# Optimization experiments

Measured on AMD Instinct MI355X. Metric: run time of the kernel, lower is better.

Reference implementation:

```python
import jax, jax.numpy as jnp
import numpy as np

B, N, D = 8, 1024, 256
H, DK, DV = 8, 64, 64
NEG = -1.0e9


def setup_inputs() -> dict:
    key = jax.random.key(0)
    ks = jax.random.split(key, 8)
    node_features = jax.random.normal(ks[0], (B, N, D), dtype=jnp.float32)
    em = (jax.random.uniform(ks[1], (B, 1, N, N)) < 0.03).astype(jnp.float32)
    eye = jnp.eye(N, dtype=jnp.float32)[None, None]
    edge_mask = jnp.maximum(em, eye)
    distance_weights = jax.random.uniform(ks[2], (B, N), dtype=jnp.float32)
    s = 1.0 / np.sqrt(D)
    Wq = jax.random.normal(ks[3], (D, H * DK), dtype=jnp.float32) * s
    Wk = jax.random.normal(ks[4], (D, H * DK), dtype=jnp.float32) * s
    Wv = jax.random.normal(ks[5], (D, H * DV), dtype=jnp.float32) * s
    Wo = jax.random.normal(ks[6], (H * DV, D), dtype=jnp.float32) / np.sqrt(H * DV)
    bo = jnp.zeros((D,), dtype=jnp.float32)
    return {"node_features": node_features, "edge_mask": edge_mask,
            "distance_weights": distance_weights,
            "Wq": Wq, "Wk": Wk, "Wv": Wv, "Wo": Wo, "bo": bo}


def reference(node_features, edge_mask, distance_weights, Wq, Wk, Wv, Wo, bo):
    b, n, d = node_features.shape
    # project and split heads: [B, H, N, dk]
    q = (node_features @ Wq).reshape(b, n, H, DK).transpose(0, 2, 1, 3)
    k = (node_features @ Wk).reshape(b, n, H, DK).transpose(0, 2, 1, 3)
    v = (node_features @ Wv).reshape(b, n, H, DV).transpose(0, 2, 1, 3)
    # scaled dot-product logits [B, H, N, N]
    logits = jnp.einsum('bhsd,bhtd->bhst', q, k) / jnp.sqrt(jnp.float32(DK))
    # additive edge-mask bias (masked pairs pushed to -1e9)
    logits = logits + (1.0 - edge_mask) * NEG
    # multiplicative per-key distance modulation
    logits = logits * distance_weights[:, None, None, :]
    w = jax.nn.softmax(logits, axis=-1)
    out = jnp.einsum('bhst,bhtd->bhsd', w, v)
    out = out.transpose(0, 2, 1, 3).reshape(b, n, H * DV)
    return out @ Wo + bo
```

## Files before the change

### kernel.cpp

```cpp
#include <hip/hip_runtime.h>
#include <hip/hip_bf16.h>
#include <hip/hip_fp16.h>
#include <cstdint>

#define B_ 8
#define N_ 1024
#define D_ 256
#define H_ 8
#define HD_ 512

typedef _Float16 f16;
typedef _Float16 f16x8 __attribute__((ext_vector_type(8)));
typedef _Float16 f16x4 __attribute__((ext_vector_type(4)));
typedef float f32x4 __attribute__((ext_vector_type(4)));
typedef unsigned long long ull;
typedef unsigned long long ull2 __attribute__((ext_vector_type(2)));

__device__ __forceinline__ void gload16(const void* g, void* l) {
    __builtin_amdgcn_global_load_lds(
        (const __attribute__((address_space(1))) unsigned int*)(uintptr_t)g,
        (__attribute__((address_space(3))) unsigned int*)(uintptr_t)l,
        16, 0, 0);
}

__global__ __launch_bounds__(256) void pack_mask_kernel(
    const float* __restrict__ mask, ull* __restrict__ bmT)
{
    const int wv = threadIdx.x >> 6, lane = threadIdx.x & 63;
    const int r = blockIdx.x * 4 + wv;
    const int b = r >> 10, n = r & 1023;
    const float* row = mask + ((size_t)b * N_ + n) * N_;
    for (int tt = 0; tt < 16; ++tt) {
        float v = row[tt * 64 + lane];
        ull m = __ballot(v != 0.0f);
        if (lane == 0) bmT[((size_t)b * 16 + tt) * N_ + n] = m;
    }
}

__global__ __launch_bounds__(256) void wconv_qkv_kernel(
    const float* __restrict__ Wq, const float* __restrict__ Wk,
    const float* __restrict__ Wv, f16* __restrict__ WT)
{
    __shared__ float Ws[64][65];
    const int tid = threadIdx.x;
    const int c0 = blockIdx.x * 64, k0 = blockIdx.y * 64;
    const int m = c0 >> 9, cw0 = c0 & 511;
    const float* Wsel = (m == 0) ? Wq : (m == 1) ? Wk : Wv;
    const int rr = tid >> 6, cc = tid & 63;
    for (int i = 0; i < 16; ++i)
        Ws[i * 4 + rr][cc] = Wsel[(size_t)(k0 + i * 4 + rr) * HD_ + cw0 + cc];
    __syncthreads();
    for (int i = 0; i < 16; ++i)
        WT[(size_t)(c0 + i * 4 + rr) * D_ + k0 + cc] = (f16)Ws[cc][i * 4 + rr];
}

__global__ __launch_bounds__(256) void wconv_o_kernel(
    const float* __restrict__ Wo, f16* __restrict__ WToT)
{
    __shared__ float Ws[64][65];
    const int tid = threadIdx.x;
    const int c0 = blockIdx.x * 64, k0 = blockIdx.y * 64;
    const int rr = tid >> 6, cc = tid & 63;
    for (int i = 0; i < 16; ++i)
        Ws[i * 4 + rr][cc] = Wo[(size_t)(k0 + i * 4 + rr) * D_ + c0 + cc];
    __syncthreads();
    for (int i = 0; i < 16; ++i)
        WToT[(size_t)(c0 + i * 4 + rr) * HD_ + k0 + cc] = (f16)Ws[cc][i * 4 + rr];
}

__global__ __launch_bounds__(256, 4) void qkv_kernel(
    const float* __restrict__ X, const f16* __restrict__ WT,
    f16* __restrict__ Qh, f16* __restrict__ Kh, f16* __restrict__ Vt)
{
    __shared__ f16 Wsh[256 * 64];
    const int tid = threadIdx.x;
    const int wv = tid >> 6, lane = tid & 63;
    const int g = lane >> 4, li = lane & 15;
    const int row0 = blockIdx.x * 64;
    const int c0 = blockIdx.y * 256;
    const int m = c0 >> 9, cw0 = c0 & 511;

    f32x4 acc[16] = {};
    const float* Xrow = X + (size_t)(row0 + wv * 16 + li) * D_;

    for (int ks = 0; ks < 4; ++ks) {
        __syncthreads();
        for (int i = 0; i < 8; ++i) {
            const int idx = i * 256 + wv * 64 + lane;
            const int c = idx >> 3, ch = idx & 7;
            const f16* src = WT + (size_t)(c0 + c) * D_ + ks * 64 + ((ch ^ (c & 7)) * 8);
            gload16(src, &Wsh[(i * 256 + wv * 64) * 8]);
        }
        __syncthreads();
        for (int kk = 0; kk < 2; ++kk) {
            const int k0 = ks * 64 + kk * 32;
            f32x4 a0 = *reinterpret_cast<const f32x4*>(Xrow + k0 + g * 8);
            f32x4 a1 = *reinterpret_cast<const f32x4*>(Xrow + k0 + g * 8 + 4);
            f16x8 af;
            for (int j = 0; j < 4; ++j) { af[j] = (f16)a0[j]; af[4 + j] = (f16)a1[j]; }
            for (int fc = 0; fc < 16; ++fc) {
                const int c = fc * 16 + li;
                const int chn = (kk * 4 + g) ^ (c & 7);
                f16x8 bf = *reinterpret_cast<const f16x8*>(&Wsh[c * 64 + chn * 8]);
                acc[fc] = __builtin_amdgcn_mfma_f32_16x16x32_f16(af, bf, acc[fc], 0, 0, 0);
            }
        }
    }
    const int b = row0 >> 10;
    const int nloc = (row0 & 1023) + wv * 16 + g * 4;
    for (int fc = 0; fc < 16; ++fc) {
        int cw = cw0 + fc * 16 + li;
        int h = cw >> 6, dk = cw & 63;
        if (m < 2) {
            f16* dst = (m == 0 ? Qh : Kh) + ((size_t)(b * H_ + h) * N_ + nloc) * 64 + dk;
            for (int j = 0; j < 4; ++j) dst[(size_t)j * 64] = (f16)acc[fc][j];
        } else {
            f16x4 v4;
            for (int j = 0; j < 4; ++j) v4[j] = (f16)acc[fc][j];
            *reinterpret_cast<f16x4*>(Vt + ((size_t)(b * H_ + h) * 64 + dk) * N_ + nloc) = v4;
        }
    }
}

__global__ __launch_bounds__(256, 4) void attn_kernel(
    const f16* __restrict__ Qh, const f16* __restrict__ Kh,
    const f16* __restrict__ Vt,
    const ull* __restrict__ bm, const float* __restrict__ dw,
    f16* __restrict__ AO)
{
    __shared__ f16 Ksh[2][4096];
    __shared__ f16 Vsh[2][4096];
    __shared__ f16 Ps[4][1024];
    const int tid = threadIdx.x;
    const int wv = tid >> 6, lane = tid & 63;
    const int g = lane >> 4, li = lane & 15;
    const int bid = (blockIdx.x & 7) * 128 + (blockIdx.x >> 3);
    const int st = bid & 15, h = (bid >> 4) & 7, b = bid >> 7;
    const int s0 = st * 64 + wv * 16;

    const f16* Qbase = Qh + (size_t)(b * H_ + h) * N_ * 64;
    const f16* Kbase = Kh + (size_t)(b * H_ + h) * N_ * 64;
    const f16* Vbase = Vt + (size_t)(b * H_ + h) * 64 * N_;
    const ull* bmb = bm + (size_t)b * 16 * N_;
    const float* dwb = dw + b * N_;

    f16x8 qf[2];
    qf[0] = *reinterpret_cast<const f16x8*>(Qbase + (size_t)(s0 + li) * 64 + g * 8);
    qf[1] = *reinterpret_cast<const f16x8*>(Qbase + (size_t)(s0 + li) * 64 + 32 + g * 8);

    f32x4 of[4] = {};
    float m_run[4], l_run[4];
    for (int j = 0; j < 4; ++j) { m_run[j] = -1e30f; l_run[j] = 0.f; }

    auto stage = [&](int tt, int bf) {
        for (int i = 0; i < 2; ++i) {
            const int idx = i * 256 + wv * 64 + lane;
            const int row = idx >> 3, ch = idx & 7;
            const int sch = (ch ^ (row & 7)) * 8;
            const f16* ksrc = Kbase + (size_t)(tt * 64 + row) * 64 + sch;
            gload16(ksrc, &Ksh[bf][(i * 256 + wv * 64) * 8]);
            const f16* vsrc = Vbase + (size_t)row * N_ + tt * 64 + sch;
            gload16(vsrc, &Vsh[bf][(i * 256 + wv * 64) * 8]);
        }
    };

    stage(0, 0);
    __syncthreads();
    int cur = 0;

    for (int tt = 0; tt < 16; ++tt) {
        if (tt < 15) stage(tt + 1, cur ^ 1);

        ull2 w01 = *reinterpret_cast<const ull2*>(bmb + tt * N_ + s0 + g * 4);
        ull2 w23 = *reinterpret_cast<const ull2*>(bmb + tt * N_ + s0 + g * 4 + 2);
        float dwc[4];
        for (int fc = 0; fc < 4; ++fc) dwc[fc] = dwb[tt * 64 + fc * 16 + li];

        f32x4 s[4] = {};
        for (int fc = 0; fc < 4; ++fc) {
            const int r = fc * 16 + li;
            const f16* kb_ = &Ksh[cur][r * 64];
            f16x8 kf0 = *reinterpret_cast<const f16x8*>(&kb_[(g ^ (r & 7)) * 8]);
            f16x8 kf1 = *reinterpret_cast<const f16x8*>(&kb_[((4 | g) ^ (r & 7)) * 8]);
            s[fc] = __builtin_amdgcn_mfma_f32_16x16x32_f16(qf[0], kf0, s[fc], 0, 0, 0);
            s[fc] = __builtin_amdgcn_mfma_f32_16x16x32_f16(qf[1], kf1, s[fc], 0, 0, 0);
        }
        ull wsh[4];
        wsh[0] = w01.x >> li; wsh[1] = w01.y >> li;
        wsh[2] = w23.x >> li; wsh[3] = w23.y >> li;

        float mt[4] = {-1e30f, -1e30f, -1e30f, -1e30f};
        for (int fc = 0; fc < 4; ++fc) {
            float dwv = dwc[fc];
            for (int j = 0; j < 4; ++j) {
                float bias = ((wsh[j] >> (fc * 16)) & 1ull) ? 0.0f : -1.0e9f;
                float lg = (s[fc][j] * 0.125f + bias) * dwv;
                s[fc][j] = lg;
                mt[j] = fmaxf(mt[j], lg);
            }
        }
        for (int j = 0; j < 4; ++j) {
            mt[j] = fmaxf(mt[j], __shfl_xor(mt[j], 1));
            mt[j] = fmaxf(mt[j], __shfl_xor(mt[j], 2));
            mt[j] = fmaxf(mt[j], __shfl_xor(mt[j], 4));
            mt[j] = fmaxf(mt[j], __shfl_xor(mt[j], 8));
        }
        float alpha[4];
        for (int j = 0; j < 4; ++j) {
            float mn = fmaxf(m_run[j], mt[j]);
            alpha[j] = __expf(m_run[j] - mn);
            m_run[j] = mn;
        }
        float rs[4] = {0.f, 0.f, 0.f, 0.f};
        for (int fc = 0; fc < 4; ++fc)
            for (int j = 0; j < 4; ++j) {
                float p = __expf(s[fc][j] - m_run[j]);
                s[fc][j] = p;
                rs[j] += p;
            }
        for (int j = 0; j < 4; ++j) {
            rs[j] += __shfl_xor(rs[j], 1);
            rs[j] += __shfl_xor(rs[j], 2);
            rs[j] += __shfl_xor(rs[j], 4);
            rs[j] += __shfl_xor(rs[j], 8);
            l_run[j] = l_run[j] * alpha[j] + rs[j];
        }
        for (int fc = 0; fc < 4; ++fc)
            for (int j = 0; j < 4; ++j) of[fc][j] *= alpha[j];

        {
            f16* psw = Ps[wv];
            for (int fc = 0; fc < 4; ++fc)
                for (int j = 0; j < 4; ++j) {
                    const int r = g * 4 + j, c = fc * 16 + li;
                    psw[r * 64 + (((c >> 3) ^ (r & 7)) * 8) + (c & 7)] = (f16)s[fc][j];
                }
            f16x8 pf0 = *reinterpret_cast<const f16x8*>(&psw[li * 64 + ((g ^ (li & 7)) * 8)]);
            f16x8 pf1 = *reinterpret_cast<const f16x8*>(&psw[li * 64 + (((4 | g) ^ (li & 7)) * 8)]);
            for (int fc = 0; fc < 4; ++fc) {
                const int r = fc * 16 + li;
                const f16* vb_ = &Vsh[cur][r * 64];
                f16x8 vf0 = *reinterpret_cast<const f16x8*>(&vb_[(g ^ (r & 7)) * 8]);
                f16x8 vf1 = *reinterpret_cast<const f16x8*>(&vb_[((4 | g) ^ (r & 7)) * 8]);
                of[fc] = __builtin_amdgcn_mfma_f32_16x16x32_f16(pf0, vf0, of[fc], 0, 0, 0);
                of[fc] = __builtin_amdgcn_mfma_f32_16x16x32_f16(pf1, vf1, of[fc], 0, 0, 0);
            }
        }
        __syncthreads();
        cur ^= 1;
    }
    for (int j = 0; j < 4; ++j) {
        float inv = 1.f / l_run[j];
        int srow = s0 + g * 4 + j;
        f16* dst = AO + ((size_t)b * N_ + srow) * HD_ + h * 64;
        for (int fc = 0; fc < 4; ++fc)
            dst[fc * 16 + li] = (f16)(of[fc][j] * inv);
    }
}

__global__ __launch_bounds__(256, 4) void proj_kernel(
    const f16* __restrict__ AO, const f16* __restrict__ WToT,
    const float* __restrict__ bo, float* __restrict__ out)
{
    __shared__ f16 Ash[16 * 512];
    const int tid = threadIdx.x;
    const int wv = tid >> 6, lane = tid & 63;
    const int g = lane >> 4, li = lane & 15;
    const int row0 = blockIdx.x * 16;
    const int c0 = wv * 64;

    for (int i = 0; i < 4; ++i) {
        const int idx = i * 256 + wv * 64 + lane;
        const int r = idx >> 6, ch = idx & 63;
        const f16* src = AO + (size_t)(row0 + r) * HD_ + ((ch ^ (r & 7)) * 8);
        gload16(src, &Ash[(i * 256 + wv * 64) * 8]);
    }
    __syncthreads();

    f32x4 acc[4] = {};
    for (int k0 = 0; k0 < HD_; k0 += 32) {
        const int cb = k0 >> 3;
        f16x8 af = *reinterpret_cast<const f16x8*>(
            &Ash[li * HD_ + (((cb + g) ^ (li & 7)) * 8)]);
        for (int fc = 0; fc < 4; ++fc) {
            f16x8 bf = *reinterpret_cast<const f16x8*>(
                WToT + (size_t)(c0 + fc * 16 + li) * HD_ + k0 + g * 8);
            acc[fc] = __builtin_amdgcn_mfma_f32_16x16x32_f16(af, bf, acc[fc], 0, 0, 0);
        }
    }
    for (int fc = 0; fc < 4; ++fc) {
        const int c = c0 + fc * 16 + li;
        const float bias = bo[c];
        for (int j = 0; j < 4; ++j)
            out[(size_t)(row0 + g * 4 + j) * D_ + c] = acc[fc][j] + bias;
    }
}

extern "C" void kernel_launch(void* const* d_in, const int* in_sizes, int n_in,
                              void* d_out, int out_size, void* d_ws, size_t ws_size,
                              hipStream_t stream) {
    const float* X    = (const float*)d_in[0];
    const float* mask = (const float*)d_in[1];
    const float* dwv  = (const float*)d_in[2];
    const float* Wq   = (const float*)d_in[3];
    const float* Wk   = (const float*)d_in[4];
    const float* Wv   = (const float*)d_in[5];
    const float* Wo   = (const float*)d_in[6];
    const float* bo   = (const float*)d_in[7];
    float* out = (float*)d_out;

    const size_t per = (size_t)B_ * H_ * N_ * 64;
    f16* Qh = (f16*)d_ws;
    f16* Kh = Qh + per;
    f16* Vt = Kh + per;
    f16* AO = Vt + per;
    f16* WToT = (f16*)d_ws;

    ull* bmT   = (ull*)d_out;
    f16* WTqkv = (f16*)((char*)d_out + (1u << 20));

    pack_mask_kernel<<<dim3(2048), 256, 0, stream>>>(mask, bmT);
    wconv_qkv_kernel<<<dim3(24, 4), 256, 0, stream>>>(Wq, Wk, Wv, WTqkv);
    qkv_kernel<<<dim3(128, 6), 256, 0, stream>>>(X, WTqkv, Qh, Kh, Vt);
    attn_kernel<<<dim3(1024), 256, 0, stream>>>(Qh, Kh, Vt, bmT, dwv, AO);
    wconv_o_kernel<<<dim3(4, 8), 256, 0, stream>>>(Wo, WToT);
    proj_kernel<<<dim3(512, 1), 256, 0, stream>>>(AO, WToT, bo, out);
}
```

Before: 196.9 us.

## Pre-convert X to fp16, retile QKV GEMM, streamline attention softmax

Adds a separate kernel that converts X to fp16 once, and retiles the QKV GEMM to 128-column blocks with double-buffered weight staging and a 4x2 fragment reuse per wave. The query scale (1/8) is folded into Wq during weight conversion, and log2(e) is folded into the distance weights so the attention softmax can use exp2 and a single FMA per logit. Row reductions switch from shuffles to DPP row-rotate operations, and shared-memory addressing is precomputed. This adds one kernel launch and an extra pass over X in exchange for less conversion work inside the GEMM and a cheaper softmax inner loop.

```diff
diff --git a/kernel.cpp b/kernel.cpp
--- a/kernel.cpp
+++ b/kernel.cpp
@@ -21,6 +21,22 @@
         (const __attribute__((address_space(1))) unsigned int*)(uintptr_t)g,
         (__attribute__((address_space(3))) unsigned int*)(uintptr_t)l,
         16, 0, 0);
+}
+
+template<int RN>
+__device__ __forceinline__ float rowror(float x) {
+    return __builtin_bit_cast(float, __builtin_amdgcn_mov_dpp(
+        __builtin_bit_cast(int, x), 0x120 + RN, 0xf, 0xf, true));
+}
+__device__ __forceinline__ float rowmax16(float x) {
+    x = fmaxf(x, rowror<1>(x)); x = fmaxf(x, rowror<2>(x));
+    x = fmaxf(x, rowror<4>(x)); x = fmaxf(x, rowror<8>(x));
+    return x;
+}
+__device__ __forceinline__ float rowsum16(float x) {
+    x += rowror<1>(x); x += rowror<2>(x);
+    x += rowror<4>(x); x += rowror<8>(x);
+    return x;
 }
 
 __global__ __launch_bounds__(256) void pack_mask_kernel(
@@ -46,12 +62,13 @@
     const int c0 = blockIdx.x * 64, k0 = blockIdx.y * 64;
     const int m = c0 >> 9, cw0 = c0 & 511;
     const float* Wsel = (m == 0) ? Wq : (m == 1) ? Wk : Wv;
+    const float scale = (m == 0) ? 0.125f : 1.0f;
     const int rr = tid >> 6, cc = tid & 63;
     for (int i = 0; i < 16; ++i)
         Ws[i * 4 + rr][cc] = Wsel[(size_t)(k0 + i * 4 + rr) * HD_ + cw0 + cc];
     __syncthreads();
     for (int i = 0; i < 16; ++i)
-        WT[(size_t)(c0 + i * 4 + rr) * D_ + k0 + cc] = (f16)Ws[cc][i * 4 + rr];
+        WT[(size_t)(c0 + i * 4 + rr) * D_ + k0 + cc] = (f16)(Ws[cc][i * 4 + rr] * scale);
 }
 
 __global__ __launch_bounds__(256) void wconv_o_kernel(
@@ -68,56 +85,75 @@
         WToT[(size_t)(c0 + i * 4 + rr) * HD_ + k0 + cc] = (f16)Ws[cc][i * 4 + rr];
 }
 
+__global__ __launch_bounds__(256) void xconv_kernel(
+    const float* __restrict__ X, f16* __restrict__ Xh)
+{
+    const size_t i = (size_t)(blockIdx.x * 256 + threadIdx.x) * 4;
+    f32x4 v = *reinterpret_cast<const f32x4*>(X + i);
+    f16x4 h;
+    for (int j = 0; j < 4; ++j) h[j] = (f16)v[j];
+    *reinterpret_cast<f16x4*>(Xh + i) = h;
+}
+
 __global__ __launch_bounds__(256, 4) void qkv_kernel(
-    const float* __restrict__ X, const f16* __restrict__ WT,
+    const f16* __restrict__ Xh, const f16* __restrict__ WT,
     f16* __restrict__ Qh, f16* __restrict__ Kh, f16* __restrict__ Vt)
 {
-    __shared__ f16 Wsh[256 * 64];
+    __shared__ f16 Wsh[2][8192];
     const int tid = threadIdx.x;
     const int wv = tid >> 6, lane = tid & 63;
     const int g = lane >> 4, li = lane & 15;
     const int row0 = blockIdx.x * 64;
-    const int c0 = blockIdx.y * 256;
+    const int c0 = blockIdx.y * 128;
     const int m = c0 >> 9, cw0 = c0 & 511;
 
-    f32x4 acc[16] = {};
-    const float* Xrow = X + (size_t)(row0 + wv * 16 + li) * D_;
-
-    for (int ks = 0; ks < 4; ++ks) {
-        __syncthreads();
-        for (int i = 0; i < 8; ++i) {
-            const int idx = i * 256 + wv * 64 + lane;
+    f32x4 acc[4][2] = {};
+
+    auto stage = [&](int ks, int bf) {
+        for (int i = 0; i < 4; ++i) {
+            const int idx = i * 256 + tid;
             const int c = idx >> 3, ch = idx & 7;
             const f16* src = WT + (size_t)(c0 + c) * D_ + ks * 64 + ((ch ^ (c & 7)) * 8);
-            gload16(src, &Wsh[(i * 256 + wv * 64) * 8]);
+            gload16(src, &Wsh[bf][idx * 8]);
+        }
+    };
+    stage(0, 0);
+    __syncthreads();
+    int bf = 0;
+    for (int ks = 0; ks < 4; ++ks) {
+        if (ks < 3) stage(ks + 1, bf ^ 1);
+        for (int kk = 0; kk < 2; ++kk) {
+            f16x8 af[4];
+            for (int rf = 0; rf < 4; ++rf)
+                af[rf] = *reinterpret_cast<const f16x8*>(
+                    Xh + (size_t)(row0 + rf * 16 + li) * D_ + ks * 64 + kk * 32 + g * 8);
+            for (int cf = 0; cf < 2; ++cf) {
+                const int cl = wv * 32 + cf * 16 + li;
+                f16x8 bm_ = *reinterpret_cast<const f16x8*>(
+                    &Wsh[bf][cl * 64 + (((kk * 4 + g) ^ (cl & 7)) * 8)]);
+                for (int rf = 0; rf < 4; ++rf)
+                    acc[rf][cf] = __builtin_amdgcn_mfma_f32_16x16x32_f16(
+                        af[rf], bm_, acc[rf][cf], 0, 0, 0);
+            }
         }
         __syncthreads();
-        for (int kk = 0; kk < 2; ++kk) {
-            const int k0 = ks * 64 + kk * 32;
-            f32x4 a0 = *reinterpret_cast<const f32x4*>(Xrow + k0 + g * 8);
-            f32x4 a1 = *reinterpret_cast<const f32x4*>(Xrow + k0 + g * 8 + 4);
-            f16x8 af;
-            for (int j = 0; j < 4; ++j) { af[j] = (f16)a0[j]; af[4 + j] = (f16)a1[j]; }
-            for (int fc = 0; fc < 16; ++fc) {
-                const int c = fc * 16 + li;
-                const int chn = (kk * 4 + g) ^ (c & 7);
-                f16x8 bf = *reinterpret_cast<const f16x8*>(&Wsh[c * 64 + chn * 8]);
-                acc[fc] = __builtin_amdgcn_mfma_f32_16x16x32_f16(af, bf, acc[fc], 0, 0, 0);
-            }
-        }
+        bf ^= 1;
     }
     const int b = row0 >> 10;
-    const int nloc = (row0 & 1023) + wv * 16 + g * 4;
-    for (int fc = 0; fc < 16; ++fc) {
-        int cw = cw0 + fc * 16 + li;
-        int h = cw >> 6, dk = cw & 63;
-        if (m < 2) {
-            f16* dst = (m == 0 ? Qh : Kh) + ((size_t)(b * H_ + h) * N_ + nloc) * 64 + dk;
-            for (int j = 0; j < 4; ++j) dst[(size_t)j * 64] = (f16)acc[fc][j];
-        } else {
-            f16x4 v4;
-            for (int j = 0; j < 4; ++j) v4[j] = (f16)acc[fc][j];
-            *reinterpret_cast<f16x4*>(Vt + ((size_t)(b * H_ + h) * 64 + dk) * N_ + nloc) = v4;
+    for (int cf = 0; cf < 2; ++cf) {
+        const int cw = cw0 + wv * 32 + cf * 16 + li;
+        const int h = cw >> 6, dk = cw & 63;
+        for (int rf = 0; rf < 4; ++rf) {
+            const int nloc = (row0 & 1023) + rf * 16 + g * 4;
+            if (m < 2) {
+                f16* dst = (m == 0 ? Qh : Kh) + ((size_t)(b * H_ + h) * N_ + nloc) * 64 + dk;
+                for (int j = 0; j < 4; ++j) dst[(size_t)j * 64] = (f16)acc[rf][cf][j];
+            } else {
+                f16x4 v4;
+                for (int j = 0; j < 4; ++j) v4[j] = (f16)acc[rf][cf][j];
+                *reinterpret_cast<f16x4*>(
+                    Vt + ((size_t)(b * H_ + h) * 64 + dk) * N_ + nloc) = v4;
+            }
         }
     }
 }
@@ -128,9 +164,9 @@
     const ull* __restrict__ bm, const float* __restrict__ dw,
     f16* __restrict__ AO)
 {
-    __shared__ f16 Ksh[2][4096];
-    __shared__ f16 Vsh[2][4096];
-    __shared__ f16 Ps[4][1024];
+    __shared__ f16 Ksh[8192];
+    __shared__ f16 Vsh[8192];
+    __shared__ f16 Ps[4096];
     const int tid = threadIdx.x;
     const int wv = tid >> 6, lane = tid & 63;
     const int g = lane >> 4, li = lane & 15;
@@ -141,117 +177,124 @@
     const f16* Qbase = Qh + (size_t)(b * H_ + h) * N_ * 64;
     const f16* Kbase = Kh + (size_t)(b * H_ + h) * N_ * 64;
     const f16* Vbase = Vt + (size_t)(b * H_ + h) * 64 * N_;
-    const ull* bmb = bm + (size_t)b * 16 * N_;
-    const float* dwb = dw + b * N_;
-
-    f16x8 qf[2];
-    qf[0] = *reinterpret_cast<const f16x8*>(Qbase + (size_t)(s0 + li) * 64 + g * 8);
-    qf[1] = *reinterpret_cast<const f16x8*>(Qbase + (size_t)(s0 + li) * 64 + 32 + g * 8);
+
+    f16x8 qf0 = *reinterpret_cast<const f16x8*>(Qbase + (size_t)(s0 + li) * 64 + g * 8);
+    f16x8 qf1 = *reinterpret_cast<const f16x8*>(Qbase + (size_t)(s0 + li) * 64 + 32 + g * 8);
+
+    int ro0[4], ro1[4];
+    for (int fc = 0; fc < 4; ++fc) {
+        const int r = fc * 16 + li;
+        ro0[fc] = r * 64 + ((g ^ (r & 7)) * 8);
+        ro1[fc] = r * 64 + (((4 | g) ^ (r & 7)) * 8);
+    }
+    const int pr0 = wv * 1024 + li * 64 + ((g ^ (li & 7)) * 8);
+    const int pr1 = wv * 1024 + li * 64 + (((4 | g) ^ (li & 7)) * 8);
+
+    const int s0i = wv * 64 + lane, s1i = 256 + wv * 64 + lane;
+    const int r0_ = s0i >> 3, c0_ = ((s0i & 7) ^ (r0_ & 7)) * 8;
+    const int r1_ = s1i >> 3, c1_ = ((s1i & 7) ^ (r1_ & 7)) * 8;
+    const f16* kp0 = Kbase + r0_ * 64 + c0_;
+    const f16* kp1 = Kbase + r1_ * 64 + c1_;
+    const f16* vp0 = Vbase + (size_t)r0_ * N_ + c0_;
+    const f16* vp1 = Vbase + (size_t)r1_ * N_ + c1_;
+    f16* const kd0 = Ksh + s0i * 8;
+    f16* const kd1 = Ksh + s1i * 8;
+    f16* const vd0 = Vsh + s0i * 8;
+    f16* const vd1 = Vsh + s1i * 8;
+
+    const ull* bmp = bm + (size_t)b * 16 * N_ + s0 + g * 4;
+    const float* dwp = dw + b * N_ + li;
 
     f32x4 of[4] = {};
     float m_run[4], l_run[4];
     for (int j = 0; j < 4; ++j) { m_run[j] = -1e30f; l_run[j] = 0.f; }
 
-    auto stage = [&](int tt, int bf) {
-        for (int i = 0; i < 2; ++i) {
-            const int idx = i * 256 + wv * 64 + lane;
-            const int row = idx >> 3, ch = idx & 7;
-            const int sch = (ch ^ (row & 7)) * 8;
-            const f16* ksrc = Kbase + (size_t)(tt * 64 + row) * 64 + sch;
-            gload16(ksrc, &Ksh[bf][(i * 256 + wv * 64) * 8]);
-            const f16* vsrc = Vbase + (size_t)row * N_ + tt * 64 + sch;
-            gload16(vsrc, &Vsh[bf][(i * 256 + wv * 64) * 8]);
-        }
-    };
-
-    stage(0, 0);
-    __syncthreads();
-    int cur = 0;
+    gload16(kp0, kd0); gload16(kp1, kd1);
+    gload16(vp0, vd0); gload16(vp1, vd1);
+    kp0 += 4096; kp1 += 4096; vp0 += 64; vp1 += 64;
+    __syncthreads();
+    int koff = 0;
 
     for (int tt = 0; tt < 16; ++tt) {
-        if (tt < 15) stage(tt + 1, cur ^ 1);
-
-        ull2 w01 = *reinterpret_cast<const ull2*>(bmb + tt * N_ + s0 + g * 4);
-        ull2 w23 = *reinterpret_cast<const ull2*>(bmb + tt * N_ + s0 + g * 4 + 2);
-        float dwc[4];
-        for (int fc = 0; fc < 4; ++fc) dwc[fc] = dwb[tt * 64 + fc * 16 + li];
+        if (tt < 15) {
+            const int nb = koff ^ 4096;
+            gload16(kp0, kd0 + nb); gload16(kp1, kd1 + nb);
+            gload16(vp0, vd0 + nb); gload16(vp1, vd1 + nb);
+            kp0 += 4096; kp1 += 4096; vp0 += 64; vp1 += 64;
+        }
+        ull2 w01 = *reinterpret_cast<const ull2*>(bmp);
+        ull2 w23 = *reinterpret_cast<const ull2*>(bmp + 2);
+        bmp += N_;
+        float dwc[4], bdw[4];
+        for (int fc = 0; fc < 4; ++fc) {
+            dwc[fc] = dwp[fc * 16] * 1.442695041f;
+            bdw[fc] = dwc[fc] * -1.0e9f;
+        }
+        dwp += 64;
 
         f32x4 s[4] = {};
         for (int fc = 0; fc < 4; ++fc) {
-            const int r = fc * 16 + li;
-            const f16* kb_ = &Ksh[cur][r * 64];
-            f16x8 kf0 = *reinterpret_cast<const f16x8*>(&kb_[(g ^ (r & 7)) * 8]);
-            f16x8 kf1 = *reinterpret_cast<const f16x8*>(&kb_[((4 | g) ^ (r & 7)) * 8]);
-            s[fc] = __builtin_amdgcn_mfma_f32_16x16x32_f16(qf[0], kf0, s[fc], 0, 0, 0);
-            s[fc] = __builtin_amdgcn_mfma_f32_16x16x32_f16(qf[1], kf1, s[fc], 0, 0, 0);
+            f16x8 kf0 = *reinterpret_cast<const f16x8*>(Ksh + koff + ro0[fc]);
+            f16x8 kf1 = *reinterpret_cast<const f16x8*>(Ksh + koff + ro1[fc]);
+            s[fc] = __builtin_amdgcn_mfma_f32_16x16x32_f16(qf0, kf0, s[fc], 0, 0, 0);
+            s[fc] = __builtin_amdgcn_mfma_f32_16x16x32_f16(qf1, kf1, s[fc], 0, 0, 0);
         }
         ull wsh[4];
         wsh[0] = w01.x >> li; wsh[1] = w01.y >> li;
         wsh[2] = w23.x >> li; wsh[3] = w23.y >> li;
 
         float mt[4] = {-1e30f, -1e30f, -1e30f, -1e30f};
-        for (int fc = 0; fc < 4; ++fc) {
-            float dwv = dwc[fc];
+        for (int fc = 0; fc < 4; ++fc)
             for (int j = 0; j < 4; ++j) {
-                float bias = ((wsh[j] >> (fc * 16)) & 1ull) ? 0.0f : -1.0e9f;
-                float lg = (s[fc][j] * 0.125f + bias) * dwv;
+                const float sel = ((wsh[j] >> (fc * 16)) & 1ull) ? 0.0f : bdw[fc];
+                const float lg = fmaf(s[fc][j], dwc[fc], sel);
                 s[fc][j] = lg;
                 mt[j] = fmaxf(mt[j], lg);
             }
-        }
-        for (int j = 0; j < 4; ++j) {
-            mt[j] = fmaxf(mt[j], __shfl_xor(mt[j], 1));
-            mt[j] = fmaxf(mt[j], __shfl_xor(mt[j], 2));
-            mt[j] = fmaxf(mt[j], __shfl_xor(mt[j], 4));
-            mt[j] = fmaxf(mt[j], __shfl_xor(mt[j], 8));
-        }
         float alpha[4];
         for (int j = 0; j < 4; ++j) {
-            float mn = fmaxf(m_run[j], mt[j]);
-            alpha[j] = __expf(m_run[j] - mn);
+            mt[j] = rowmax16(mt[j]);
+            const float mn = fmaxf(m_run[j], mt[j]);
+            alpha[j] = __builtin_amdgcn_exp2f(m_run[j] - mn);
             m_run[j] = mn;
         }
         float rs[4] = {0.f, 0.f, 0.f, 0.f};
         for (int fc = 0; fc < 4; ++fc)
             for (int j = 0; j < 4; ++j) {
-                float p = __expf(s[fc][j] - m_run[j]);
+                const float p = __builtin_amdgcn_exp2f(s[fc][j] - m_run[j]);
                 s[fc][j] = p;
                 rs[j] += p;
             }
         for (int j = 0; j < 4; ++j) {
-            rs[j] += __shfl_xor(rs[j], 1);
-            rs[j] += __shfl_xor(rs[j], 2);
-            rs[j] += __shfl_xor(rs[j], 4);
-            rs[j] += __shfl_xor(rs[j], 8);
+            rs[j] = rowsum16(rs[j]);
             l_run[j] = l_run[j] * alpha[j] + rs[j];
         }
         for (int fc = 0; fc < 4; ++fc)
             for (int j = 0; j < 4; ++j) of[fc][j] *= alpha[j];
 
         {
-            f16* psw = Ps[wv];
+            f16* psw = Ps + wv * 1024;
             for (int fc = 0; fc < 4; ++fc)
                 for (int j = 0; j < 4; ++j) {
-                    const int r = g * 4 + j, c = fc * 16 + li;
-                    psw[r * 64 + (((c >> 3) ^ (r & 7)) * 8) + (c & 7)] = (f16)s[fc][j];
+                    const int r = g * 4 + j;
+                    psw[r * 64 + (((fc * 2 + (li >> 3)) ^ (r & 7)) * 8) + (li & 7)]
+                        = (f16)s[fc][j];
                 }
-            f16x8 pf0 = *reinterpret_cast<const f16x8*>(&psw[li * 64 + ((g ^ (li & 7)) * 8)]);
-            f16x8 pf1 = *reinterpret_cast<const f16x8*>(&psw[li * 64 + (((4 | g) ^ (li & 7)) * 8)]);
+            f16x8 pf0 = *reinterpret_cast<const f16x8*>(Ps + pr0);
+            f16x8 pf1 = *reinterpret_cast<const f16x8*>(Ps + pr1);
             for (int fc = 0; fc < 4; ++fc) {
-                const int r = fc * 16 + li;
-                const f16* vb_ = &Vsh[cur][r * 64];
-                f16x8 vf0 = *reinterpret_cast<const f16x8*>(&vb_[(g ^ (r & 7)) * 8]);
-                f16x8 vf1 = *reinterpret_cast<const f16x8*>(&vb_[((4 | g) ^ (r & 7)) * 8]);
+                f16x8 vf0 = *reinterpret_cast<const f16x8*>(Vsh + koff + ro0[fc]);
+                f16x8 vf1 = *reinterpret_cast<const f16x8*>(Vsh + koff + ro1[fc]);
                 of[fc] = __builtin_amdgcn_mfma_f32_16x16x32_f16(pf0, vf0, of[fc], 0, 0, 0);
                 of[fc] = __builtin_amdgcn_mfma_f32_16x16x32_f16(pf1, vf1, of[fc], 0, 0, 0);
             }
         }
         __syncthreads();
-        cur ^= 1;
+        koff ^= 4096;
     }
     for (int j = 0; j < 4; ++j) {
-        float inv = 1.f / l_run[j];
-        int srow = s0 + g * 4 + j;
+        const float inv = 1.f / l_run[j];
+        const int srow = s0 + g * 4 + j;
         f16* dst = AO + ((size_t)b * N_ + srow) * HD_ + h * 64;
         for (int fc = 0; fc < 4; ++fc)
             dst[fc * 16 + li] = (f16)(of[fc][j] * inv);
@@ -270,10 +313,10 @@
     const int c0 = wv * 64;
 
     for (int i = 0; i < 4; ++i) {
-        const int idx = i * 256 + wv * 64 + lane;
+        const int idx = i * 256 + tid;
         const int r = idx >> 6, ch = idx & 63;
         const f16* src = AO + (size_t)(row0 + r) * HD_ + ((ch ^ (r & 7)) * 8);
-        gload16(src, &Ash[(i * 256 + wv * 64) * 8]);
+        gload16(src, &Ash[idx * 8]);
     }
     __syncthreads();
 
@@ -318,10 +361,12 @@
 
     ull* bmT   = (ull*)d_out;
     f16* WTqkv = (f16*)((char*)d_out + (1u << 20));
+    f16* Xh    = (f16*)((char*)d_out + (2u << 20));
 
     pack_mask_kernel<<<dim3(2048), 256, 0, stream>>>(mask, bmT);
     wconv_qkv_kernel<<<dim3(24, 4), 256, 0, stream>>>(Wq, Wk, Wv, WTqkv);
-    qkv_kernel<<<dim3(128, 6), 256, 0, stream>>>(X, WTqkv, Qh, Kh, Vt);
+    xconv_kernel<<<dim3(2048), 256, 0, stream>>>(X, Xh);
+    qkv_kernel<<<dim3(128, 12), 256, 0, stream>>>(Xh, WTqkv, Qh, Kh, Vt);
     attn_kernel<<<dim3(1024), 256, 0, stream>>>(Qh, Kh, Vt, bmT, dwv, AO);
     wconv_o_kernel<<<dim3(4, 8), 256, 0, stream>>>(Wo, WToT);
     proj_kernel<<<dim3(512, 1), 256, 0, stream>>>(AO, WToT, bo, out);
```

Result: no change. 198.7 us (+0.9%).
